# Optimization experiments

Measured on AMD Instinct MI355X. Metric: run time of the kernel, lower is better.

The kernel has to match this reference:

```python
import jax, jax.numpy as jnp
import numpy as np

DIM = 1024
H = 16
HD = DIM // H  # 64
K = 256


def setup_inputs() -> dict:
    key = jax.random.key(0)
    ks = jax.random.split(key, 8)
    x = jax.random.normal(ks[0], (4, 4096, DIM), dtype=jnp.float32)
    # torch nn.Linear weights are (out, in); y = x @ W.T
    Wq = jax.random.normal(ks[1], (DIM, DIM), dtype=jnp.float32) * (DIM ** -0.5)
    Wk = jax.random.normal(ks[2], (DIM, DIM), dtype=jnp.float32) * (DIM ** -0.5)
    Wv = jax.random.normal(ks[3], (DIM, DIM), dtype=jnp.float32) * (DIM ** -0.5)
    E = jax.random.normal(ks[4], (K, HD), dtype=jnp.float32)
    F = jax.random.normal(ks[5], (K, HD), dtype=jnp.float32)
    Wo = jax.random.normal(ks[6], (DIM, DIM), dtype=jnp.float32) * (DIM ** -0.5)
    bo = jax.random.normal(ks[7], (DIM,), dtype=jnp.float32) * 0.01
    return {"x": x, "Wq": Wq, "Wk": Wk, "Wv": Wv, "E": E, "F": F, "Wo": Wo, "bo": bo}


def reference(x, Wq, Wk, Wv, E, F, Wo, bo):
    B, N, D = x.shape
    d = HD
    q = (x @ Wq.T).reshape(B, N, H, d).transpose(0, 2, 1, 3)  # (B,H,N,d)
    k = (x @ Wk.T).reshape(B, N, H, d).transpose(0, 2, 1, 3)
    v = (x @ Wv.T).reshape(B, N, H, d).transpose(0, 2, 1, 3)
    # Faithful to source: einsum contracts over n (sequence), elementwise in d.
    k_proj = jnp.einsum('bhnd,kd->bhkd', k, E)  # (B,H,K,d)
    v_proj = jnp.einsum('bhnd,kd->bhkd', v, F)
    attn = jnp.einsum('bhnd,bhkd->bhnk', q, k_proj) / (d ** 0.5)  # (B,H,N,K)
    attn = jax.nn.softmax(attn, axis=-1)
    out = jnp.einsum('bhnk,bhkd->bhnd', attn, v_proj)
    out = out.transpose(0, 2, 1, 3).reshape(B, N, D)
    return out @ Wo.T + bo
```

## Files before the change

### kernel.cpp

```cpp
#include <hip/hip_runtime.h>

#define DIM 1024
#define BATCH 4
#define SEQ 4096
#define NH 16
#define HD 64
#define KP 256

typedef float f32x4 __attribute__((ext_vector_type(4)));
typedef _Float16 half8 __attribute__((ext_vector_type(8)));

__device__ __forceinline__ void gll16(const void* g, void* l) {
  __builtin_amdgcn_global_load_lds(
      (const __attribute__((address_space(1))) void*)g,
      (__attribute__((address_space(3))) void*)l, 16, 0, 0);
}

#define DPPF(v, ctrl)                                                        \
  __builtin_bit_cast(float, __builtin_amdgcn_mov_dpp(                        \
                                __builtin_bit_cast(int, v), ctrl, 0xF, 0xF, true))

__global__ void k_cvt(const float* __restrict__ s, _Float16* __restrict__ d) {
  int i = (blockIdx.x * 256 + threadIdx.x) * 8;
  f32x4 a = *(const f32x4*)(s + i);
  f32x4 b = *(const f32x4*)(s + i + 4);
  half8 h;
  h[0] = a[0]; h[1] = a[1]; h[2] = a[2]; h[3] = a[3];
  h[4] = b[0]; h[5] = b[1]; h[6] = b[2]; h[7] = b[3];
  *(half8*)(d + i) = h;
}

__global__ void k_cvtw(const float* __restrict__ Wq, const float* __restrict__ Wo,
                       _Float16* __restrict__ Wq_h, _Float16* __restrict__ Wo_h) {
  int bb = blockIdx.x;
  const float* s = (bb < 512) ? Wq : Wo;
  _Float16* d = (bb < 512) ? Wq_h : Wo_h;
  int i = ((bb & 511) * 256 + threadIdx.x) * 8;
  f32x4 a = *(const f32x4*)(s + i);
  f32x4 b = *(const f32x4*)(s + i + 4);
  half8 h;
  h[0] = a[0]; h[1] = a[1]; h[2] = a[2]; h[3] = a[3];
  h[4] = b[0]; h[5] = b[1]; h[6] = b[2]; h[7] = b[3];
  *(half8*)(d + i) = h;
}

__global__ void k_misc(const float* __restrict__ E, const float* __restrict__ F,
                       _Float16* __restrict__ E_h, _Float16* __restrict__ Ft,
                       float* __restrict__ xsum) {
  int bb = blockIdx.x;
  if (bb < 16) {
    xsum[bb * 256 + threadIdx.x] = 0.f;
  } else if (bb < 24) {
    int i = ((bb - 16) * 256 + threadIdx.x) * 8;
    f32x4 a = *(const f32x4*)(E + i);
    f32x4 b = *(const f32x4*)(E + i + 4);
    half8 h;
    h[0] = a[0]; h[1] = a[1]; h[2] = a[2]; h[3] = a[3];
    h[4] = b[0]; h[5] = b[1]; h[6] = b[2]; h[7] = b[3];
    *(half8*)(E_h + i) = h;
  } else {
    int i = (bb - 24) * 256 + threadIdx.x;
    int k = i >> 6, d = i & 63;
    Ft[d * KP + (k & 15) * 16 + (k >> 4)] = (_Float16)F[i];
  }
}

__global__ void k_xsum(const _Float16* __restrict__ xh, float* __restrict__ xs) {
  int c = blockIdx.x * 256 + threadIdx.x;
  int b = blockIdx.y;
  int n0 = blockIdx.z * 128;
  const _Float16* p = xh + (size_t)(b * SEQ + n0) * DIM + c;
  float s = 0.f;
  #pragma unroll 8
  for (int i = 0; i < 128; i++) s += (float)p[i * DIM];
  atomicAdd(&xs[b * DIM + c], s);
}

__global__ void k_sksv(const float* __restrict__ xs, const float* __restrict__ Wk,
                       const float* __restrict__ Wv, float* __restrict__ Sk,
                       float* __restrict__ Sv) {
  int idx = blockIdx.x * 4 + (threadIdx.x >> 6);
  int lane = threadIdx.x & 63;
  int kv = idx >> 12;
  int rem = idx & 4095;
  int b = rem >> 10, c = rem & 1023;
  const float* W = (kv ? Wv : Wk) + c * DIM;
  const float* xp = xs + b * DIM;
  float a = 0.f;
  #pragma unroll
  for (int i = 0; i < 16; i++) a += xp[lane + i * 64] * W[lane + i * 64];
  for (int off = 32; off; off >>= 1) a += __shfl_down(a, off);
  if (lane == 0) (kv ? Sv : Sk)[rem] = a;
}

template <int MODE>
__global__ __launch_bounds__(256) void k_gemm(const _Float16* __restrict__ A,
                                              const _Float16* __restrict__ Bw,
                                              void* __restrict__ Cout,
                                              const float* __restrict__ sb) {
  __shared__ _Float16 sh[2][128 * 32];
  _Float16* As = sh[0];
  _Float16* Bs = sh[1];
  const int tid = threadIdx.x;
  const int w = tid >> 6, lane = tid & 63;
  const int m0 = blockIdx.x * 128, n0 = blockIdx.y * 128;
  const int q4 = lane >> 4, mm = lane & 15;
  const int wm = w & 1, wn = w >> 1;
  f32x4 acc[4][4] = {};
  const _Float16* Ag = A + (m0 + w * 32 + (lane >> 2)) * DIM + (lane & 3) * 8;
  const _Float16* Bg = Bw + (n0 + w * 32 + (lane >> 2)) * DIM + (lane & 3) * 8;
  _Float16* AsW = As + w * 1024;
  _Float16* BsW = Bs + w * 1024;
  for (int k0 = 0; k0 < DIM; k0 += 32) {
    gll16(Ag + k0, AsW);
    gll16(Ag + k0 + 16 * DIM, AsW + 512);
    gll16(Bg + k0, BsW);
    gll16(Bg + k0 + 16 * DIM, BsW + 512);
    __syncthreads();
    half8 av[4], bv[4];
    const _Float16* Ap = As + (wm * 64 + mm) * 32 + q4 * 8;
    const _Float16* Bp = Bs + (wn * 64 + mm) * 32 + q4 * 8;
    #pragma unroll
    for (int t = 0; t < 4; t++) {
      av[t] = *(const half8*)(Ap + t * 512);
      bv[t] = *(const half8*)(Bp + t * 512);
    }
    #pragma unroll
    for (int mt = 0; mt < 4; mt++)
      #pragma unroll
      for (int nt = 0; nt < 4; nt++)
        acc[mt][nt] = __builtin_amdgcn_mfma_f32_16x16x32_f16(av[mt], bv[nt], acc[mt][nt], 0, 0, 0);
    __syncthreads();
  }
  if (MODE == 0) {
    _Float16* Lh = (_Float16*)sh;
    #pragma unroll
    for (int p = 0; p < 2; p++) {
      if (wm == p) {
        #pragma unroll
        for (int nt = 0; nt < 4; nt++) {
          int cl = wn * 64 + nt * 16 + mm;
          float s = sb[(m0 >> 12) * DIM + n0 + cl] * (0.125f * 1.44269504088896f);
          #pragma unroll
          for (int mt = 0; mt < 4; mt++) {
            int rl = mt * 16 + q4 * 4;
            #pragma unroll
            for (int r = 0; r < 4; r++)
              Lh[(rl + r) * 128 + cl] = (_Float16)(acc[mt][nt][r] * s);
          }
        }
      }
      __syncthreads();
      int row_l = tid >> 2, c0 = (tid & 3) * 32;
      _Float16* dst = (_Float16*)Cout + (size_t)(m0 + p * 64 + row_l) * DIM + n0 + c0;
      #pragma unroll
      for (int i = 0; i < 4; i++)
        *(half8*)(dst + i * 8) = *(half8*)(Lh + row_l * 128 + c0 + i * 8);
      __syncthreads();
    }
  } else {
    float* Lf = (float*)sh;
    #pragma unroll
    for (int p = 0; p < 4; p++) {
      if (wm == (p >> 1)) {
        #pragma unroll
        for (int nt = 0; nt < 4; nt++) {
          int cl = wn * 64 + nt * 16 + mm;
          float s = sb[n0 + cl];
          #pragma unroll
          for (int mti = 0; mti < 2; mti++) {
            int mt = (p & 1) * 2 + mti;
            int rl = mt * 16 + q4 * 4 - (p & 1) * 32;
            #pragma unroll
            for (int r = 0; r < 4; r++)
              Lf[(rl + r) * 128 + cl] = acc[mt][nt][r] + s;
          }
        }
      }
      __syncthreads();
      int row_l = tid >> 3, c0 = (tid & 7) * 16;
      float* dst = (float*)Cout + (size_t)(m0 + p * 32 + row_l) * DIM + n0 + c0;
      #pragma unroll
      for (int i = 0; i < 4; i++)
        *(f32x4*)(dst + i * 4) = *(f32x4*)(Lf + row_l * 128 + c0 + i * 4);
      __syncthreads();
    }
  }
}

__global__ __launch_bounds__(256) void k_attn(const _Float16* __restrict__ Q,
                                              const _Float16* __restrict__ E,
                                              const _Float16* __restrict__ Ftp,
                                              const float* __restrict__ Sv,
                                              _Float16* __restrict__ O) {
  __shared__ _Float16 Ps[4][16][264];
  const int tid = threadIdx.x;
  const int w = tid >> 6, lane = tid & 63;
  const int q4 = lane >> 4, mm = lane & 15;
  const int bh = blockIdx.y;
  const int b = bh >> 4, h = bh & 15;
  const int row_base = blockIdx.x * 512 + w * 128;

  half8 ef[16][2];
  #pragma unroll
  for (int t = 0; t < 16; t++)
    #pragma unroll
    for (int kk = 0; kk < 2; kk++)
      ef[t][kk] = *(const half8*)(E + (t * 16 + mm) * HD + kk * 32 + q4 * 8);
  half8 ff[4][8];
  #pragma unroll
  for (int nt = 0; nt < 4; nt++)
    #pragma unroll
    for (int kk = 0; kk < 8; kk++)
      ff[nt][kk] = *(const half8*)(Ftp + (nt * 16 + mm) * KP + kk * 32 + q4 * 8);
  float sv[4];
  #pragma unroll
  for (int nt = 0; nt < 4; nt++) sv[nt] = Sv[b * DIM + h * HD + nt * 16 + mm];

  const _Float16* Qbase = Q + ((size_t)(b * SEQ + row_base + mm)) * DIM + h * HD + q4 * 8;
  half8 qa0 = *(const half8*)(Qbase);
  half8 qa1 = *(const half8*)(Qbase + 32);

  for (int tile = 0; tile < 8; tile++) {
    f32x4 acc[16] = {};
    #pragma unroll
    for (int t = 0; t < 16; t++)
      acc[t] = __builtin_amdgcn_mfma_f32_16x16x32_f16(qa0, ef[t][0], acc[t], 0, 0, 0);
    #pragma unroll
    for (int t = 0; t < 16; t++)
      acc[t] = __builtin_amdgcn_mfma_f32_16x16x32_f16(qa1, ef[t][1], acc[t], 0, 0, 0);
    half8 qn0, qn1;
    if (tile < 7) {
      const _Float16* Qn = Qbase + (size_t)(tile + 1) * 16 * DIM;
      qn0 = *(const half8*)(Qn);
      qn1 = *(const half8*)(Qn + 32);
    }
    float mx[4] = {-1e30f, -1e30f, -1e30f, -1e30f};
    #pragma unroll
    for (int t = 0; t < 16; t++)
      #pragma unroll
      for (int r = 0; r < 4; r++) mx[r] = fmaxf(mx[r], acc[t][r]);
    #pragma unroll
    for (int r = 0; r < 4; r++) {
      float m = mx[r];
      m = fmaxf(m, DPPF(m, 0x121));
      m = fmaxf(m, DPPF(m, 0x122));
      m = fmaxf(m, DPPF(m, 0x124));
      m = fmaxf(m, DPPF(m, 0x128));
      mx[r] = m;
    }
    float sm[4] = {0.f, 0.f, 0.f, 0.f};
    #pragma unroll
    for (int t = 0; t < 16; t++)
      #pragma unroll
      for (int r = 0; r < 4; r++) {
        float p = __builtin_amdgcn_exp2f(acc[t][r] - mx[r]);
        acc[t][r] = p;
        sm[r] += p;
      }
    #pragma unroll
    for (int r = 0; r < 4; r++) {
      float s = sm[r];
      s += DPPF(s, 0x121);
      s += DPPF(s, 0x122);
      s += DPPF(s, 0x124);
      s += DPPF(s, 0x128);
      sm[r] = 1.f / s;
    }
    #pragma unroll
    for (int r = 0; r < 4; r++) {
      half8 h0, h1;
      #pragma unroll
      for (int t = 0; t < 8; t++) h0[t] = (_Float16)acc[t][r];
      #pragma unroll
      for (int t = 0; t < 8; t++) h1[t] = (_Float16)acc[t + 8][r];
      *(half8*)&Ps[w][q4 * 4 + r][mm * 16] = h0;
      *(half8*)&Ps[w][q4 * 4 + r][mm * 16 + 8] = h1;
    }
    f32x4 acc2[4] = {};
    #pragma unroll
    for (int kk = 0; kk < 8; kk++) {
      half8 pa = *(const half8*)&Ps[w][mm][kk * 32 + q4 * 8];
      #pragma unroll
      for (int nt = 0; nt < 4; nt++)
        acc2[nt] = __builtin_amdgcn_mfma_f32_16x16x32_f16(pa, ff[nt][kk], acc2[nt], 0, 0, 0);
    }
    const int rw0 = row_base + tile * 16;
    #pragma unroll
    for (int nt = 0; nt < 4; nt++)
      #pragma unroll
      for (int r = 0; r < 4; r++)
        O[(size_t)(b * SEQ + rw0 + q4 * 4 + r) * DIM + h * HD + nt * 16 + mm] =
            (_Float16)(acc2[nt][r] * (sm[r] * sv[nt]));
    qa0 = qn0;
    qa1 = qn1;
  }
}

extern "C" void kernel_launch(void* const* d_in, const int* in_sizes, int n_in,
                              void* d_out, int out_size, void* d_ws, size_t ws_size,
                              hipStream_t stream) {
  (void)in_sizes; (void)n_in; (void)out_size; (void)ws_size;
  const float* x  = (const float*)d_in[0];
  const float* Wq = (const float*)d_in[1];
  const float* Wk = (const float*)d_in[2];
  const float* Wv = (const float*)d_in[3];
  const float* E  = (const float*)d_in[4];
  const float* F  = (const float*)d_in[5];
  const float* Wo = (const float*)d_in[6];
  const float* bo = (const float*)d_in[7];
  char* ws = (char*)d_ws;
  _Float16* x_h  = (_Float16*)(ws);
  _Float16* O_h  = (_Float16*)(ws);
  _Float16* Q_h  = (_Float16*)(ws + 33554432);
  _Float16* Wq_h = (_Float16*)(ws + 67108864);
  _Float16* Wo_h = (_Float16*)(ws + 69206016);
  _Float16* E_h  = (_Float16*)(ws + 71303168);
  _Float16* Ft_h = (_Float16*)(ws + 71335936);
  float* xsum    = (float*)(ws + 71368704);
  float* Sk      = (float*)(ws + 71385088);
  float* Sv      = (float*)(ws + 71401472);
  float* out     = (float*)d_out;

  k_cvt<<<8192, 256, 0, stream>>>(x, x_h);
  k_misc<<<88, 256, 0, stream>>>(E, F, E_h, Ft_h, xsum);
  k_cvtw<<<1024, 256, 0, stream>>>(Wq, Wo, Wq_h, Wo_h);
  k_xsum<<<dim3(4, BATCH, 32), 256, 0, stream>>>(x_h, xsum);
  k_sksv<<<2048, 256, 0, stream>>>(xsum, Wk, Wv, Sk, Sv);
  k_gemm<0><<<dim3(128, 8), 256, 0, stream>>>(x_h, Wq_h, (void*)Q_h, Sk);
  k_attn<<<dim3(8, 64), 256, 0, stream>>>(Q_h, E_h, Ft_h, Sv, O_h);
  k_gemm<1><<<dim3(128, 8), 256, 0, stream>>>(O_h, Wo_h, (void*)out, bo);
}
```

Baseline: 314.1 us.

## Pipeline GEMM with triple-buffered LDS, fuse x conversion with column sum, fold Sk into E

The GEMM main loop now uses a three-stage LDS ring with XOR-swizzled layout, inline ds_read_b128 and explicit vmcnt waits, so global loads overlap MFMA work. Epilogue LDS strides are padded to reduce bank conflicts. The x fp32-to-fp16 conversion is fused with the sequence column sum, so x_h is no longer re-read. The small prep kernels are merged into one launch. The Sk and softmax scaling moves out of the Q GEMM epilogue and is folded into the E fragments inside the attention kernel. This adds hand-tuned asm scheduling that is fragile, and it changes where fp16 rounding happens.

```diff
diff --git a/kernel.cpp b/kernel.cpp
--- a/kernel.cpp
+++ b/kernel.cpp
@@ -9,6 +9,8 @@
 
 typedef float f32x4 __attribute__((ext_vector_type(4)));
 typedef _Float16 half8 __attribute__((ext_vector_type(8)));
+typedef _Float16 half4v __attribute__((ext_vector_type(4)));
+typedef int i32x4 __attribute__((ext_vector_type(4)));
 
 __device__ __forceinline__ void gll16(const void* g, void* l) {
   __builtin_amdgcn_global_load_lds(
@@ -16,64 +18,71 @@
       (__attribute__((address_space(3))) void*)l, 16, 0, 0);
 }
 
+__device__ __forceinline__ unsigned lds_addr(const void* p) {
+  return (unsigned)(size_t)(const __attribute__((address_space(3))) void*)p;
+}
+
+#define DSR128(dst, base, imm)                                               \
+  asm volatile("ds_read_b128 %0, %1 offset:" #imm : "=&v"(dst) : "v"(base))
+
+#define BARR __builtin_amdgcn_s_barrier()
+#define LGKM0                                                                \
+  do {                                                                       \
+    asm volatile("s_waitcnt lgkmcnt(0)" ::: "memory");                       \
+    __builtin_amdgcn_sched_barrier(0);                                       \
+  } while (0)
+#define VMC(n) asm volatile("s_waitcnt vmcnt(" #n ")" ::: "memory")
+
 #define DPPF(v, ctrl)                                                        \
   __builtin_bit_cast(float, __builtin_amdgcn_mov_dpp(                        \
                                 __builtin_bit_cast(int, v), ctrl, 0xF, 0xF, true))
 
-__global__ void k_cvt(const float* __restrict__ s, _Float16* __restrict__ d) {
-  int i = (blockIdx.x * 256 + threadIdx.x) * 8;
-  f32x4 a = *(const f32x4*)(s + i);
-  f32x4 b = *(const f32x4*)(s + i + 4);
-  half8 h;
-  h[0] = a[0]; h[1] = a[1]; h[2] = a[2]; h[3] = a[3];
-  h[4] = b[0]; h[5] = b[1]; h[6] = b[2]; h[7] = b[3];
-  *(half8*)(d + i) = h;
-}
-
-__global__ void k_cvtw(const float* __restrict__ Wq, const float* __restrict__ Wo,
-                       _Float16* __restrict__ Wq_h, _Float16* __restrict__ Wo_h) {
-  int bb = blockIdx.x;
-  const float* s = (bb < 512) ? Wq : Wo;
-  _Float16* d = (bb < 512) ? Wq_h : Wo_h;
-  int i = ((bb & 511) * 256 + threadIdx.x) * 8;
-  f32x4 a = *(const f32x4*)(s + i);
-  f32x4 b = *(const f32x4*)(s + i + 4);
-  half8 h;
-  h[0] = a[0]; h[1] = a[1]; h[2] = a[2]; h[3] = a[3];
-  h[4] = b[0]; h[5] = b[1]; h[6] = b[2]; h[7] = b[3];
-  *(half8*)(d + i) = h;
-}
-
-__global__ void k_misc(const float* __restrict__ E, const float* __restrict__ F,
-                       _Float16* __restrict__ E_h, _Float16* __restrict__ Ft,
-                       float* __restrict__ xsum) {
+__global__ void k_pre(const float* __restrict__ Wq, const float* __restrict__ Wo,
+                      const float* __restrict__ F, _Float16* __restrict__ Wq_h,
+                      _Float16* __restrict__ Wo_h, _Float16* __restrict__ Ft,
+                      float* __restrict__ xsum) {
   int bb = blockIdx.x;
   if (bb < 16) {
     xsum[bb * 256 + threadIdx.x] = 0.f;
-  } else if (bb < 24) {
-    int i = ((bb - 16) * 256 + threadIdx.x) * 8;
-    f32x4 a = *(const f32x4*)(E + i);
-    f32x4 b = *(const f32x4*)(E + i + 4);
+  } else if (bb < 80) {
+    int i = (bb - 16) * 256 + threadIdx.x;
+    int k = i >> 6, d = i & 63;
+    Ft[d * KP + (k & 15) * 16 + (k >> 4)] = (_Float16)F[i];
+  } else {
+    int b2 = bb - 80;
+    const float* s = (b2 < 512) ? Wq : Wo;
+    _Float16* d = (b2 < 512) ? Wq_h : Wo_h;
+    int i = ((b2 & 511) * 256 + threadIdx.x) * 8;
+    f32x4 a = *(const f32x4*)(s + i);
+    f32x4 b = *(const f32x4*)(s + i + 4);
     half8 h;
     h[0] = a[0]; h[1] = a[1]; h[2] = a[2]; h[3] = a[3];
     h[4] = b[0]; h[5] = b[1]; h[6] = b[2]; h[7] = b[3];
-    *(half8*)(E_h + i) = h;
-  } else {
-    int i = (bb - 24) * 256 + threadIdx.x;
-    int k = i >> 6, d = i & 63;
-    Ft[d * KP + (k & 15) * 16 + (k >> 4)] = (_Float16)F[i];
-  }
-}
-
-__global__ void k_xsum(const _Float16* __restrict__ xh, float* __restrict__ xs) {
-  int c = blockIdx.x * 256 + threadIdx.x;
-  int b = blockIdx.y;
-  int n0 = blockIdx.z * 128;
-  const _Float16* p = xh + (size_t)(b * SEQ + n0) * DIM + c;
-  float s = 0.f;
-  #pragma unroll 8
-  for (int i = 0; i < 128; i++) s += (float)p[i * DIM];
-  atomicAdd(&xs[b * DIM + c], s);
+    *(half8*)(d + i) = h;
+  }
+}
+
+__global__ void k_xcvt(const float* __restrict__ x, _Float16* __restrict__ xh,
+                       float* __restrict__ xs) {
+  const int b = blockIdx.y, r0 = blockIdx.x * 32;
+  const int c0 = threadIdx.x * 4;
+  const float* p = x + ((size_t)(b * SEQ + r0)) * DIM + c0;
+  _Float16* q = xh + ((size_t)(b * SEQ + r0)) * DIM + c0;
+  float s0 = 0.f, s1 = 0.f, s2 = 0.f, s3 = 0.f;
+  #pragma unroll 4
+  for (int i = 0; i < 32; i++) {
+    f32x4 v = *(const f32x4*)(p + (size_t)i * DIM);
+    s0 += v[0]; s1 += v[1]; s2 += v[2]; s3 += v[3];
+    half4v hv;
+    hv[0] = (_Float16)v[0]; hv[1] = (_Float16)v[1];
+    hv[2] = (_Float16)v[2]; hv[3] = (_Float16)v[3];
+    *(half4v*)(q + (size_t)i * DIM) = hv;
+  }
+  float* xp = xs + b * DIM + c0;
+  atomicAdd(xp + 0, s0);
+  atomicAdd(xp + 1, s1);
+  atomicAdd(xp + 2, s2);
+  atomicAdd(xp + 3, s3);
 }
 
 __global__ void k_sksv(const float* __restrict__ xs, const float* __restrict__ Wk,
@@ -93,45 +102,79 @@
   if (lane == 0) (kv ? Sv : Sk)[rem] = a;
 }
 
+#define MF(X, Y, C)                                                          \
+  __builtin_amdgcn_mfma_f32_16x16x32_f16(__builtin_bit_cast(half8, (X)),     \
+                                         __builtin_bit_cast(half8, (Y)),     \
+                                         (C), 0, 0, 0)
+
+#define STAGE(RB, T)                                                         \
+  do {                                                                       \
+    gll16(Ag + (T) * 32, &sh[RB][0][sdst]);                                  \
+    gll16(Ag + (T) * 32 + 64 * DIM, &sh[RB][0][sdst + 2048]);                \
+    gll16(Bg + (T) * 32, &sh[RB][1][sdst]);                                  \
+    gll16(Bg + (T) * 32 + 64 * DIM, &sh[RB][1][sdst + 2048]);                \
+  } while (0)
+
+#define GT(T, SLOT, SS, STEN, VM)                                            \
+  {                                                                          \
+    const unsigned ab = a0 + (SLOT) * 16384u;                                \
+    const unsigned bb = b0 + (SLOT) * 16384u;                                \
+    i32x4 fa0, fa1, fa2, fa3, fb0, fb1, fb2, fb3;                            \
+    DSR128(fb0, bb, 0); DSR128(fb1, bb, 1024);                               \
+    DSR128(fb2, bb, 2048); DSR128(fb3, bb, 3072);                            \
+    DSR128(fa0, ab, 0); DSR128(fa1, ab, 1024);                               \
+    DSR128(fa2, ab, 2048); DSR128(fa3, ab, 3072);                            \
+    if (STEN) { STAGE(SS, (T) + 2); }                                        \
+    LGKM0;                                                                   \
+    __builtin_amdgcn_s_setprio(1);                                           \
+    acc[0][0] = MF(fa0, fb0, acc[0][0]); acc[0][1] = MF(fa0, fb1, acc[0][1]);\
+    acc[0][2] = MF(fa0, fb2, acc[0][2]); acc[0][3] = MF(fa0, fb3, acc[0][3]);\
+    acc[1][0] = MF(fa1, fb0, acc[1][0]); acc[1][1] = MF(fa1, fb1, acc[1][1]);\
+    acc[1][2] = MF(fa1, fb2, acc[1][2]); acc[1][3] = MF(fa1, fb3, acc[1][3]);\
+    acc[2][0] = MF(fa2, fb0, acc[2][0]); acc[2][1] = MF(fa2, fb1, acc[2][1]);\
+    acc[2][2] = MF(fa2, fb2, acc[2][2]); acc[2][3] = MF(fa2, fb3, acc[2][3]);\
+    acc[3][0] = MF(fa3, fb0, acc[3][0]); acc[3][1] = MF(fa3, fb1, acc[3][1]);\
+    acc[3][2] = MF(fa3, fb2, acc[3][2]); acc[3][3] = MF(fa3, fb3, acc[3][3]);\
+    __builtin_amdgcn_s_setprio(0);                                           \
+    if ((VM) == 0) { VMC(4); } else if ((VM) == 1) { VMC(0); }               \
+    BARR;                                                                    \
+  }
+
 template <int MODE>
-__global__ __launch_bounds__(256) void k_gemm(const _Float16* __restrict__ A,
-                                              const _Float16* __restrict__ Bw,
-                                              void* __restrict__ Cout,
-                                              const float* __restrict__ sb) {
-  __shared__ _Float16 sh[2][128 * 32];
-  _Float16* As = sh[0];
-  _Float16* Bs = sh[1];
+__global__ __launch_bounds__(256, 3) void k_gemm(const _Float16* __restrict__ A,
+                                                 const _Float16* __restrict__ Bw,
+                                                 void* __restrict__ Cout,
+                                                 const float* __restrict__ sb) {
+  __shared__ _Float16 sh[3][2][4096];
   const int tid = threadIdx.x;
-  const int w = tid >> 6, lane = tid & 63;
+  const int w = tid >> 6, l = tid & 63;
+  const int q4 = l >> 4, mm = l & 15;
+  const int wm = w & 1, wn = w >> 1;
   const int m0 = blockIdx.x * 128, n0 = blockIdx.y * 128;
-  const int q4 = lane >> 4, mm = lane & 15;
-  const int wm = w & 1, wn = w >> 1;
   f32x4 acc[4][4] = {};
-  const _Float16* Ag = A + (m0 + w * 32 + (lane >> 2)) * DIM + (lane & 3) * 8;
-  const _Float16* Bg = Bw + (n0 + w * 32 + (lane >> 2)) * DIM + (lane & 3) * 8;
-  _Float16* AsW = As + w * 1024;
-  _Float16* BsW = Bs + w * 1024;
-  for (int k0 = 0; k0 < DIM; k0 += 32) {
-    gll16(Ag + k0, AsW);
-    gll16(Ag + k0 + 16 * DIM, AsW + 512);
-    gll16(Bg + k0, BsW);
-    gll16(Bg + k0 + 16 * DIM, BsW + 512);
-    __syncthreads();
-    half8 av[4], bv[4];
-    const _Float16* Ap = As + (wm * 64 + mm) * 32 + q4 * 8;
-    const _Float16* Bp = Bs + (wn * 64 + mm) * 32 + q4 * 8;
-    #pragma unroll
-    for (int t = 0; t < 4; t++) {
-      av[t] = *(const half8*)(Ap + t * 512);
-      bv[t] = *(const half8*)(Bp + t * 512);
-    }
-    #pragma unroll
-    for (int mt = 0; mt < 4; mt++)
-      #pragma unroll
-      for (int nt = 0; nt < 4; nt++)
-        acc[mt][nt] = __builtin_amdgcn_mfma_f32_16x16x32_f16(av[mt], bv[nt], acc[mt][nt], 0, 0, 0);
-    __syncthreads();
-  }
+
+  const int schunk = ((l & 3) ^ ((l >> 3) & 3)) * 8;
+  const _Float16* Ag = A + (size_t)(m0 + w * 16 + (l >> 2)) * DIM + schunk;
+  const _Float16* Bg = Bw + (size_t)(n0 + w * 16 + (l >> 2)) * DIM + schunk;
+  const int sdst = w * 512;
+  const int csw = (q4 ^ ((mm >> 1) & 3)) * 8;
+  const unsigned shb = lds_addr(&sh[0][0][0]);
+  const unsigned a0 = shb + (unsigned)(((wm * 64 + mm) * 32 + csw) * 2);
+  const unsigned b0 = shb + 8192u + (unsigned)(((wn * 64 + mm) * 32 + csw) * 2);
+
+  STAGE(0, 0);
+  STAGE(1, 1);
+  VMC(4);
+  BARR;
+
+  for (int tt = 0; tt < 30; tt += 3) {
+    GT(tt + 0, 0, 2, 1, 0)
+    GT(tt + 1, 1, 0, 1, 0)
+    GT(tt + 2, 2, 1, 1, 0)
+  }
+  GT(30, 0, 0, 0, 1)
+  GT(31, 1, 0, 0, 2)
+
   if (MODE == 0) {
     _Float16* Lh = (_Float16*)sh;
     #pragma unroll
@@ -139,23 +182,22 @@
       if (wm == p) {
         #pragma unroll
         for (int nt = 0; nt < 4; nt++) {
-          int cl = wn * 64 + nt * 16 + mm;
-          float s = sb[(m0 >> 12) * DIM + n0 + cl] * (0.125f * 1.44269504088896f);
+          const int cl = wn * 64 + nt * 16 + mm;
           #pragma unroll
           for (int mt = 0; mt < 4; mt++) {
-            int rl = mt * 16 + q4 * 4;
+            const int rl = mt * 16 + q4 * 4;
             #pragma unroll
             for (int r = 0; r < 4; r++)
-              Lh[(rl + r) * 128 + cl] = (_Float16)(acc[mt][nt][r] * s);
+              Lh[(rl + r) * 136 + cl] = (_Float16)acc[mt][nt][r];
           }
         }
       }
       __syncthreads();
-      int row_l = tid >> 2, c0 = (tid & 3) * 32;
+      const int row_l = tid >> 2, c0 = (tid & 3) * 32;
       _Float16* dst = (_Float16*)Cout + (size_t)(m0 + p * 64 + row_l) * DIM + n0 + c0;
       #pragma unroll
       for (int i = 0; i < 4; i++)
-        *(half8*)(dst + i * 8) = *(half8*)(Lh + row_l * 128 + c0 + i * 8);
+        *(half8*)(dst + i * 8) = *(half8*)(Lh + row_l * 136 + c0 + i * 8);
       __syncthreads();
     }
   } else {
@@ -165,32 +207,33 @@
       if (wm == (p >> 1)) {
         #pragma unroll
         for (int nt = 0; nt < 4; nt++) {
-          int cl = wn * 64 + nt * 16 + mm;
-          float s = sb[n0 + cl];
+          const int cl = wn * 64 + nt * 16 + mm;
+          const float s = sb[n0 + cl];
           #pragma unroll
           for (int mti = 0; mti < 2; mti++) {
-            int mt = (p & 1) * 2 + mti;
-            int rl = mt * 16 + q4 * 4 - (p & 1) * 32;
+            const int mt = (p & 1) * 2 + mti;
+            const int rl = mt * 16 + q4 * 4 - (p & 1) * 32;
             #pragma unroll
             for (int r = 0; r < 4; r++)
-              Lf[(rl + r) * 128 + cl] = acc[mt][nt][r] + s;
+              Lf[(rl + r) * 132 + cl] = acc[mt][nt][r] + s;
           }
         }
       }
       __syncthreads();
-      int row_l = tid >> 3, c0 = (tid & 7) * 16;
+      const int row_l = tid >> 3, c0 = (tid & 7) * 16;
       float* dst = (float*)Cout + (size_t)(m0 + p * 32 + row_l) * DIM + n0 + c0;
       #pragma unroll
       for (int i = 0; i < 4; i++)
-        *(f32x4*)(dst + i * 4) = *(f32x4*)(Lf + row_l * 128 + c0 + i * 4);
+        *(f32x4*)(dst + i * 4) = *(f32x4*)(Lf + row_l * 132 + c0 + i * 4);
       __syncthreads();
     }
   }
 }
 
 __global__ __launch_bounds__(256) void k_attn(const _Float16* __restrict__ Q,
-                                              const _Float16* __restrict__ E,
+                                              const float* __restrict__ E,
                                               const _Float16* __restrict__ Ftp,
+                                              const float* __restrict__ Sk,
                                               const float* __restrict__ Sv,
                                               _Float16* __restrict__ O) {
   __shared__ _Float16 Ps[4][16][264];
@@ -201,12 +244,34 @@
   const int b = bh >> 4, h = bh & 15;
   const int row_base = blockIdx.x * 512 + w * 128;
 
+  const float qsc = 0.125f * 1.44269504088896f;
+  float skf[2][8];
+  #pragma unroll
+  for (int kk = 0; kk < 2; kk++) {
+    f32x4 u = *(const f32x4*)(Sk + b * DIM + h * HD + kk * 32 + q4 * 8);
+    f32x4 v = *(const f32x4*)(Sk + b * DIM + h * HD + kk * 32 + q4 * 8 + 4);
+    #pragma unroll
+    for (int j = 0; j < 4; j++) {
+      skf[kk][j] = u[j] * qsc;
+      skf[kk][j + 4] = v[j] * qsc;
+    }
+  }
   half8 ef[16][2];
   #pragma unroll
   for (int t = 0; t < 16; t++)
     #pragma unroll
-    for (int kk = 0; kk < 2; kk++)
-      ef[t][kk] = *(const half8*)(E + (t * 16 + mm) * HD + kk * 32 + q4 * 8);
+    for (int kk = 0; kk < 2; kk++) {
+      const float* ep = E + (t * 16 + mm) * HD + kk * 32 + q4 * 8;
+      f32x4 e0 = *(const f32x4*)ep;
+      f32x4 e1 = *(const f32x4*)(ep + 4);
+      half8 hv;
+      #pragma unroll
+      for (int j = 0; j < 4; j++) {
+        hv[j] = (_Float16)(e0[j] * skf[kk][j]);
+        hv[j + 4] = (_Float16)(e1[j] * skf[kk][j + 4]);
+      }
+      ef[t][kk] = hv;
+    }
   half8 ff[4][8];
   #pragma unroll
   for (int nt = 0; nt < 4; nt++)
@@ -315,19 +380,16 @@
   _Float16* Q_h  = (_Float16*)(ws + 33554432);
   _Float16* Wq_h = (_Float16*)(ws + 67108864);
   _Float16* Wo_h = (_Float16*)(ws + 69206016);
-  _Float16* E_h  = (_Float16*)(ws + 71303168);
   _Float16* Ft_h = (_Float16*)(ws + 71335936);
   float* xsum    = (float*)(ws + 71368704);
   float* Sk      = (float*)(ws + 71385088);
   float* Sv      = (float*)(ws + 71401472);
   float* out     = (float*)d_out;
 
-  k_cvt<<<8192, 256, 0, stream>>>(x, x_h);
-  k_misc<<<88, 256, 0, stream>>>(E, F, E_h, Ft_h, xsum);
-  k_cvtw<<<1024, 256, 0, stream>>>(Wq, Wo, Wq_h, Wo_h);
-  k_xsum<<<dim3(4, BATCH, 32), 256, 0, stream>>>(x_h, xsum);
+  k_pre<<<1104, 256, 0, stream>>>(Wq, Wo, F, Wq_h, Wo_h, Ft_h, xsum);
+  k_xcvt<<<dim3(128, BATCH), 256, 0, stream>>>(x, x_h, xsum);
   k_sksv<<<2048, 256, 0, stream>>>(xsum, Wk, Wv, Sk, Sv);
-  k_gemm<0><<<dim3(128, 8), 256, 0, stream>>>(x_h, Wq_h, (void*)Q_h, Sk);
-  k_attn<<<dim3(8, 64), 256, 0, stream>>>(Q_h, E_h, Ft_h, Sv, O_h);
+  k_gemm<0><<<dim3(128, 8), 256, 0, stream>>>(x_h, Wq_h, (void*)Q_h, nullptr);
+  k_attn<<<dim3(8, 64), 256, 0, stream>>>(Q_h, E, Ft_h, Sk, Sv, O_h);
   k_gemm<1><<<dim3(128, 8), 256, 0, stream>>>(O_h, Wo_h, (void*)out, bo);
 }
```

After: 313.8 us. Within noise of the previous version (-0.1%).
